# Optimization experiments

Measured on AMD Instinct MI355X. Metric: run time of the kernel, lower is better.

The kernel has to match this reference:

```python
import jax, jax.numpy as jnp
import numpy as np

# scipy.ndimage.gaussian_filter(sigma=1, truncate=4): radius 4, 9-tap kernel on EVERY axis
_R = 4
_xk = np.arange(-_R, _R + 1)
_wk = np.exp(-0.5 * _xk * _xk)
_W1D = (_wk / _wk.sum()).astype(np.float32)


def _sym_idx(n, r):
    # scipy 'reflect' (symmetric, edge repeated) extension indices for any r, any n
    p = np.arange(-r, n + r)
    q = np.mod(p, 2 * n)
    return np.where(q < n, q, 2 * n - 1 - q)


def gauss_filter(x):
    # separable sigma=1 Gaussian over ALL axes (incl. batch & channel), as scipy does
    w = jnp.asarray(_W1D)
    for axis in range(x.ndim):
        n = x.shape[axis]
        idx = jnp.asarray(_sym_idx(n, _R))
        xp = jnp.take(x, idx, axis=axis)  # symmetric-padded along `axis`
        acc = w[0] * jax.lax.slice_in_dim(xp, 0, n, axis=axis)
        for k in range(1, 2 * _R + 1):
            acc = acc + w[k] * jax.lax.slice_in_dim(xp, k, k + n, axis=axis)
        x = acc
    return x


def downsample(x):
    return x[:, :, ::2, ::2, ::2]


def upsample(x):
    # faithful to source: zero-interleave D and H, but zeros are APPENDED along W
    B, C, D, H, W = x.shape
    t = jnp.stack([x, jnp.zeros_like(x)], axis=3).reshape(B, C, 2 * D, H, W)
    t = jnp.stack([t, jnp.zeros_like(t)], axis=4).reshape(B, C, 2 * D, 2 * H, W)
    t = jnp.concatenate([t, jnp.zeros_like(t)], axis=4)  # (B,C,2D,2H,2W), 2nd W-half zero
    return gauss_filter(t * 8.0)


def lap_pyramid(img, max_levels):
    pyr = []
    cur = img
    for _ in range(max_levels):
        filt = gauss_filter(cur)
        down = downsample(filt)
        up = upsample(down)
        pyr.append(cur - up)
        cur = down
    return pyr


def setup_inputs():
    key = jax.random.key(0)
    k1, k2 = jax.random.split(key)
    shape = (2, 1, 64, 256, 256)
    return {
        "input": jax.random.normal(k1, shape, dtype=jnp.float32),
        "target": jax.random.normal(k2, shape, dtype=jnp.float32),
    }


def reference(input, target):
    max_levels = 5
    pyr_in = lap_pyramid(input, max_levels)
    pyr_tg = lap_pyramid(target, max_levels)
    loss = jnp.float32(0.0)
    for a, b in zip(pyr_in, pyr_tg):
        loss = loss + jnp.mean(jnp.abs(a - b))  # F.l1_loss (mean reduction)
    return loss
```

## Files before the change

### kernel.cpp

```cpp
#include <hip/hip_runtime.h>
#include <hip/hip_bf16.h>
#include <math.h>


struct GW { float w[9]; float A, B; };

__device__ __forceinline__ int ridx(int p, int n) {
    int m = 2 * n;
    int q = (p + m) & (m - 1);
    return (q < n) ? q : (m - 1 - q);
}

__device__ __forceinline__ float block_sum256(float v) {
    #pragma unroll
    for (int off = 32; off > 0; off >>= 1) v += __shfl_down(v, off, 64);
    __shared__ float wp[4];
    int tid = threadIdx.x;
    if ((tid & 63) == 0) wp[tid >> 6] = v;
    __syncthreads();
    return wp[0] + wp[1] + wp[2] + wp[3];
}

__device__ __forceinline__ float block_sum1024(float v) {
    #pragma unroll
    for (int off = 32; off > 0; off >>= 1) v += __shfl_down(v, off, 64);
    __shared__ float wp[16];
    int tid = threadIdx.x;
    if ((tid & 63) == 0) wp[tid >> 6] = v;
    __syncthreads();
    float t = 0.f;
    if (tid == 0) {
        #pragma unroll
        for (int w = 0; w < 16; ++w) t += wp[w];
    }
    return t;
}

template<bool WDIFF>
__global__ __launch_bounds__(256)
void k1l0(const float* __restrict__ in, const float* __restrict__ tg,
          float* __restrict__ T1, __hip_bfloat16* __restrict__ DIFF,
          float* __restrict__ P, GW g)
{
    const int H = 256, W = 256, Wd = 128;
    const int x0d = blockIdx.x * 64, y0d = blockIdx.y * 16, slice = blockIdx.z;
    __shared__ float raw[40][136];
    __shared__ float mid[40][64];
    const size_t in_off  = (size_t)slice * H * W;
    const size_t out_off = (size_t)slice * 128 * 128;
    const int tid = threadIdx.x;
    const int gy0 = 2*y0d - 4, gx0 = 2*x0d - 4;
    for (int i = tid; i < 40*32; i += 256) {
        int rr = i >> 5, c4 = (i & 31) + 1;
        int gy = ridx(gy0 + rr, H);
        size_t base = in_off + (size_t)gy * W + gx0 + 4*c4;
        float4 v = *(const float4*)(in + base);
        float4 b = *(const float4*)(tg + base);
        v.x -= b.x; v.y -= b.y; v.z -= b.z; v.w -= b.w;
        *(float4*)&raw[rr][4*c4] = v;
    }
    for (int i = tid; i < 40*8; i += 256) {
        int rr = i >> 3, j = i & 7;
        int cc = (j < 4) ? j : (128 + j);
        int gy = ridx(gy0 + rr, H);
        int gx = ridx(gx0 + cc, W);
        size_t idx = in_off + (size_t)gy * W + gx;
        raw[rr][cc] = in[idx] - tg[idx];
    }
    __syncthreads();
    if (WDIFF) {
        if (blockIdx.x == 0) {
            for (int i = tid; i < 32*128; i += 256) {
                int r = i >> 7, c = i & 127;
                DIFF[in_off + (size_t)(2*y0d + r) * W + c] =
                    __float2bfloat16(raw[4 + r][4 + c]);
            }
        } else {
            for (int i = tid; i < 32*4; i += 256) {
                int r = i >> 2, c = i & 3;
                DIFF[in_off + (size_t)(2*y0d + r) * W + 128 + c] =
                    __float2bfloat16(raw[4 + r][4 + c]);
            }
        }
    }
    if (blockIdx.x == 1) {
        float lsum = 0.f;
        for (int i = tid; i < 32*124; i += 256) {
            int r = i / 124, c = i - r*124;
            lsum += fabsf(raw[4 + r][8 + c]);
        }
        float tot = block_sum256(lsum);
        if (tid == 0)
            P[blockIdx.y + 8*blockIdx.z] = tot * (1.f / 8388608.f);
    }
    for (int i = tid; i < 40*64; i += 256) {
        int rr = i >> 6, c = i & 63;
        float s = 0.f;
        #pragma unroll
        for (int k = 0; k < 9; ++k) s = fmaf(g.w[k], raw[rr][2*c + k], s);
        mid[rr][c] = s;
    }
    __syncthreads();
    {
        int r = tid >> 6, c = tid & 63;
        int ox = x0d + c;
        #pragma unroll
        for (int j = 0; j < 4; ++j) {
            int oy = y0d + r*4 + j;
            int rb = 2*(r*4 + j);
            float s = 0.f;
            #pragma unroll
            for (int k = 0; k < 9; ++k) s = fmaf(g.w[k], mid[rb + k][c], s);
            T1[out_off + (size_t)oy * Wd + ox] = s;
        }
    }
}

__device__ void dev_k2_elem(long i, const float4* __restrict__ T, float4* __restrict__ O,
                            int D, int Dd, int M4, const GW& g)
{
    if (i >= (long)Dd * M4) return;
    int zd = (int)(i / M4);
    int q  = (int)(i - (long)zd * M4);
    float4 s0 = {0,0,0,0}, s1 = {0,0,0,0};
    #pragma unroll
    for (int k = 0; k < 9; ++k) {
        int zp = 2*zd - 4 + k;
        int zk = (zp >= 0 && zp < D) ? zp : ridx(zp, D);
        float4 a = T[(size_t)zk * M4 + q];
        float4 b = T[(size_t)(D + zk) * M4 + q];
        s0.x = fmaf(g.w[k], a.x, s0.x); s0.y = fmaf(g.w[k], a.y, s0.y);
        s0.z = fmaf(g.w[k], a.z, s0.z); s0.w = fmaf(g.w[k], a.w, s0.w);
        s1.x = fmaf(g.w[k], b.x, s1.x); s1.y = fmaf(g.w[k], b.y, s1.y);
        s1.z = fmaf(g.w[k], b.z, s1.z); s1.w = fmaf(g.w[k], b.w, s1.w);
    }
    float4 o0, o1;
    o0.x = g.A*s0.x + g.B*s1.x; o0.y = g.A*s0.y + g.B*s1.y;
    o0.z = g.A*s0.z + g.B*s1.z; o0.w = g.A*s0.w + g.B*s1.w;
    o1.x = g.B*s0.x + g.A*s1.x; o1.y = g.B*s0.y + g.A*s1.y;
    o1.z = g.B*s0.z + g.A*s1.z; o1.w = g.B*s0.w + g.A*s1.w;
    O[(size_t)zd * M4 + q] = o0;
    O[(size_t)(Dd + zd) * M4 + q] = o1;
}

__global__ __launch_bounds__(256)
void k2s(const float* __restrict__ Tin, float* __restrict__ Cout,
         int D, int Dd, int M4, GW g)
{
    long i = (long)blockIdx.x * 256 + threadIdx.x;
    dev_k2_elem(i, (const float4*)Tin, (float4*)Cout, D, Dd, M4, g);
}

__device__ void dev_k1_slice(const float* __restrict__ inA, float* __restrict__ out,
                             int x0d, int y0d, int slice, int H, int W, int Hd, int Wd,
                             const GW& g)
{
    __shared__ float raw[40][136];
    __shared__ float mid[40][64];
    const size_t in_off  = (size_t)slice * H * W;
    const size_t out_off = (size_t)slice * Hd * Wd;
    const int tid = threadIdx.x;
    const int gy0 = 2*y0d - 4, gx0 = 2*x0d - 4;
    if (2*x0d + 127 < W) {
        for (int i = tid; i < 40*32; i += 256) {
            int rr = i >> 5, c4 = (i & 31) + 1;
            int gy = ridx(gy0 + rr, H);
            *(float4*)&raw[rr][4*c4] =
                *(const float4*)(inA + in_off + (size_t)gy * W + gx0 + 4*c4);
        }
        for (int i = tid; i < 40*8; i += 256) {
            int rr = i >> 3, j = i & 7;
            int cc = (j < 4) ? j : (128 + j);
            int gy = ridx(gy0 + rr, H), gx = ridx(gx0 + cc, W);
            raw[rr][cc] = inA[in_off + (size_t)gy * W + gx];
        }
    } else {
        for (int i = tid; i < 40*136; i += 256) {
            int rr = i / 136, cc = i - rr*136;
            int gy = ridx(gy0 + rr, H), gx = ridx(gx0 + cc, W);
            raw[rr][cc] = inA[in_off + (size_t)gy * W + gx];
        }
    }
    __syncthreads();
    for (int i = tid; i < 40*64; i += 256) {
        int rr = i >> 6, c = i & 63;
        float s = 0.f;
        #pragma unroll
        for (int k = 0; k < 9; ++k) s = fmaf(g.w[k], raw[rr][2*c + k], s);
        mid[rr][c] = s;
    }
    __syncthreads();
    {
        int r = tid >> 6, c = tid & 63;
        int ox = x0d + c;
        #pragma unroll
        for (int j = 0; j < 4; ++j) {
            int oy = y0d + r*4 + j;
            if (oy < Hd && ox < Wd) {
                int rb = 2*(r*4 + j);
                float s = 0.f;
                #pragma unroll
                for (int k = 0; k < 9; ++k) s = fmaf(g.w[k], mid[rb + k][c], s);
                out[out_off + (size_t)oy * Wd + ox] = s;
            }
        }
    }
}

__device__ void dev_k3_elem(long i, const float4* __restrict__ Dn, float4* __restrict__ O,
                            int D, int Dd, int M4, const GW& g)
{
    if (i >= (long)D * M4) return;
    int z = (int)(i / M4);
    int q = (int)(i - (long)z * M4);
    float4 s0 = {0,0,0,0}, s1 = {0,0,0,0};
    auto f4 = [](float4& a, float w, const float4 b) {
        a.x = fmaf(w, b.x, a.x); a.y = fmaf(w, b.y, a.y);
        a.z = fmaf(w, b.z, a.z); a.w = fmaf(w, b.w, a.w);
    };
    if (z >= 4 && z + 4 < D) {
        if ((z & 1) == 0) {
            int base = (z >> 1) - 2;
            #pragma unroll
            for (int kk = 0; kk < 5; ++kk) {
                f4(s0, g.w[2*kk], Dn[(size_t)(base + kk) * M4 + q]);
                f4(s1, g.w[2*kk], Dn[(size_t)(Dd + base + kk) * M4 + q]);
            }
        } else {
            int base = (z - 3) >> 1;
            #pragma unroll
            for (int kk = 0; kk < 4; ++kk) {
                f4(s0, g.w[2*kk+1], Dn[(size_t)(base + kk) * M4 + q]);
                f4(s1, g.w[2*kk+1], Dn[(size_t)(Dd + base + kk) * M4 + q]);
            }
        }
    } else {
        #pragma unroll
        for (int k = 0; k < 9; ++k) {
            int zk = ridx(z - 4 + k, D);
            if (!(zk & 1)) {
                int j = zk >> 1;
                f4(s0, g.w[k], Dn[(size_t)j * M4 + q]);
                f4(s1, g.w[k], Dn[(size_t)(Dd + j) * M4 + q]);
            }
        }
    }
    float4 o0, o1;
    o0.x = 8.f*(g.A*s0.x + g.B*s1.x); o0.y = 8.f*(g.A*s0.y + g.B*s1.y);
    o0.z = 8.f*(g.A*s0.z + g.B*s1.z); o0.w = 8.f*(g.A*s0.w + g.B*s1.w);
    o1.x = 8.f*(g.B*s0.x + g.A*s1.x); o1.y = 8.f*(g.B*s0.y + g.A*s1.y);
    o1.z = 8.f*(g.B*s0.z + g.A*s1.z); o1.w = 8.f*(g.B*s0.w + g.A*s1.w);
    O[(size_t)z * M4 + q] = o0;
    O[(size_t)(D + z) * M4 + q] = o1;
}

__device__ void dev_k4v0(int local, const float* __restrict__ V0,
                         const __hip_bfloat16* __restrict__ DIFF,
                         const float* __restrict__ in, const float* __restrict__ tg,
                         int use_diff, float* __restrict__ P, const GW& g)
{
    __shared__ float vt[20][72];
    __shared__ float mid[20][64];
    const int H = 256, W = 256, Hd = 128, Wd = 128, Md = 128*128;
    const int s = local / 24;
    const int rem = local - s*24;
    const int ty = rem / 3, tx = rem - ty*3;
    const int x0 = tx*64, y0 = ty*32;
    const int tid = threadIdx.x;
    const int vy0 = (y0 >> 1) - 2;
    const size_t v_off = (size_t)s * Md;
    for (int i = tid; i < 20*72; i += 256) {
        int rr = i / 72, cc = i - rr*72;
        int vy = vy0 + rr;
        int txx = x0 - 4 + cc;
        if (txx < 0) txx = -1 - txx;
        float v = 0.f;
        if (vy >= 0 && vy < Hd && txx < Wd) v = V0[v_off + (size_t)vy * Wd + txx];
        vt[rr][cc] = v;
    }
    __syncthreads();
    for (int i = tid; i < 20*64; i += 256) {
        int rr = i >> 6, c = i & 63;
        float sv = 0.f;
        #pragma unroll
        for (int k = 0; k < 9; ++k) sv = fmaf(g.w[k], vt[rr][c + k], sv);
        mid[rr][c] = sv;
    }
    __syncthreads();
    const bool yin = (y0 >= 4) && (y0 + 35 < H);
    const int c = tid & 63;
    const int ry_base = (tid >> 6) * 8;
    const int ox = x0 + c;
    const size_t c_off = (size_t)s * H * W;
    float lsum = 0.f;
    #pragma unroll
    for (int j = 0; j < 8; ++j) {
        int ry = ry_base + j;
        int oy = y0 + ry;
        if (ox < 132 && oy < H) {
            float sv = 0.f;
            if (yin) {
                if (!(j & 1)) {
                    int r0 = ry >> 1;
                    sv = g.w[0]*mid[r0][c] + g.w[2]*mid[r0+1][c] + g.w[4]*mid[r0+2][c]
                       + g.w[6]*mid[r0+3][c] + g.w[8]*mid[r0+4][c];
                } else {
                    int r0 = ((ry - 3) >> 1) + 2;
                    sv = g.w[1]*mid[r0][c] + g.w[3]*mid[r0+1][c]
                       + g.w[5]*mid[r0+2][c] + g.w[7]*mid[r0+3][c];
                }
            } else {
                #pragma unroll
                for (int k = 0; k < 9; ++k) {
                    int gy = ridx(oy - 4 + k, H);
                    if (!(gy & 1)) sv = fmaf(g.w[k], mid[(gy >> 1) - vy0][c], sv);
                }
            }
            size_t idx = c_off + (size_t)oy * W + ox;
            float cv = use_diff ? __bfloat162float(DIFF[idx]) : (in[idx] - tg[idx]);
            lsum += fabsf(cv - sv);
        }
    }
    float tot = block_sum256(lsum);
    if (tid == 0) P[1024 + local] = tot * (1.f / 8388608.f);
}

__device__ void dev_k4f(int local, const float* __restrict__ dnb,
                        const float* __restrict__ cur, float* __restrict__ Pslot,
                        int D, int H, int ntx, int nty, float invn, const GW& g)
{
    __shared__ float vt[20][72];
    __shared__ float mid[20][64];
    const int W = H, Dd = D >> 1, Hd = H >> 1, Wd = W >> 1, Md = Hd * Wd;
    const int s = local / (ntx*nty);
    const int rem = local - s*(ntx*nty);
    const int ty = rem / ntx, tx = rem - ty*ntx;
    const int x0 = tx*64, y0 = ty*32;
    const int b = s / D, z = s - b*D;
    const float* dn0 = dnb + (size_t)b * Dd * Md;
    const float* dn1 = dnb + (size_t)(1 - b) * Dd * Md;
    const int tid = threadIdx.x;
    const int vy0 = (y0 >> 1) - 2;

    const bool zin = (z >= 4) && (z + 4 < D);
    if (zin && !(z & 1)) {
        const int j0 = (z >> 1) - 2;
        for (int i = tid; i < 20*72; i += 256) {
            int rr = i / 72, cc = i - rr*72;
            int vy = vy0 + rr;
            int txx = x0 - 4 + cc;
            if (txx < 0) txx = -1 - txx;
            float v = 0.f;
            if (vy >= 0 && vy < Hd && txx < Wd) {
                size_t o = (size_t)vy * Wd + txx;
                float s0 = 0.f, s1 = 0.f;
                #pragma unroll
                for (int t = 0; t < 5; ++t) {
                    s0 = fmaf(g.w[2*t], dn0[(size_t)(j0 + t) * Md + o], s0);
                    s1 = fmaf(g.w[2*t], dn1[(size_t)(j0 + t) * Md + o], s1);
                }
                v = 8.f * (g.A*s0 + g.B*s1);
            }
            vt[rr][cc] = v;
        }
    } else if (zin) {
        const int j0 = (z - 3) >> 1;
        for (int i = tid; i < 20*72; i += 256) {
            int rr = i / 72, cc = i - rr*72;
            int vy = vy0 + rr;
            int txx = x0 - 4 + cc;
            if (txx < 0) txx = -1 - txx;
            float v = 0.f;
            if (vy >= 0 && vy < Hd && txx < Wd) {
                size_t o = (size_t)vy * Wd + txx;
                float s0 = 0.f, s1 = 0.f;
                #pragma unroll
                for (int t = 0; t < 4; ++t) {
                    s0 = fmaf(g.w[2*t+1], dn0[(size_t)(j0 + t) * Md + o], s0);
                    s1 = fmaf(g.w[2*t+1], dn1[(size_t)(j0 + t) * Md + o], s1);
                }
                v = 8.f * (g.A*s0 + g.B*s1);
            }
            vt[rr][cc] = v;
        }
    } else {
        for (int i = tid; i < 20*72; i += 256) {
            int rr = i / 72, cc = i - rr*72;
            int vy = vy0 + rr;
            int txx = x0 - 4 + cc;
            if (txx < 0) txx = -1 - txx;
            float v = 0.f;
            if (vy >= 0 && vy < Hd && txx < Wd) {
                size_t o = (size_t)vy * Wd + txx;
                float s0 = 0.f, s1 = 0.f;
                #pragma unroll
                for (int k = 0; k < 9; ++k) {
                    int zk = ridx(z - 4 + k, D);
                    if (!(zk & 1)) {
                        int j = zk >> 1;
                        s0 = fmaf(g.w[k], dn0[(size_t)j * Md + o], s0);
                        s1 = fmaf(g.w[k], dn1[(size_t)j * Md + o], s1);
                    }
                }
                v = 8.f * (g.A*s0 + g.B*s1);
            }
            vt[rr][cc] = v;
        }
    }
    __syncthreads();
    for (int i = tid; i < 20*64; i += 256) {
        int rr = i >> 6, c = i & 63;
        float sv = 0.f;
        #pragma unroll
        for (int k = 0; k < 9; ++k) sv = fmaf(g.w[k], vt[rr][c + k], sv);
        mid[rr][c] = sv;
    }
    __syncthreads();
    const bool yin = (y0 >= 4) && (y0 + 35 < H);
    const int c = tid & 63;
    const int ry_base = (tid >> 6) * 8;
    const int ox = x0 + c;
    const size_t c_off = (size_t)s * H * W;
    float lsum = 0.f;
    #pragma unroll
    for (int j = 0; j < 8; ++j) {
        int ry = ry_base + j;
        int oy = y0 + ry;
        if (ox < W && oy < H) {
            float sv = 0.f;
            if (yin) {
                if (!(j & 1)) {
                    int r0 = ry >> 1;
                    sv = g.w[0]*mid[r0][c] + g.w[2]*mid[r0+1][c] + g.w[4]*mid[r0+2][c]
                       + g.w[6]*mid[r0+3][c] + g.w[8]*mid[r0+4][c];
                } else {
                    int r0 = ((ry - 3) >> 1) + 2;
                    sv = g.w[1]*mid[r0][c] + g.w[3]*mid[r0+1][c]
                       + g.w[5]*mid[r0+2][c] + g.w[7]*mid[r0+3][c];
                }
            } else {
                #pragma unroll
                for (int k = 0; k < 9; ++k) {
                    int gy = ridx(oy - 4 + k, H);
                    if (!(gy & 1)) sv = fmaf(g.w[k], mid[(gy >> 1) - vy0][c], sv);
                }
            }
            lsum += fabsf(cur[c_off + (size_t)oy * W + ox] - sv);
        }
    }
    float tot = block_sum256(lsum);
    if (tid == 0) Pslot[local] = tot * invn;
}

__global__ __launch_bounds__(256)
void kD3(const float* __restrict__ C1, float* __restrict__ Tl1,
         float* __restrict__ V0, GW g)
{
    int bid = (int)blockIdx.x;
    if (bid < 256) {
        int ty = bid & 3, slice = bid >> 2;
        dev_k1_slice(C1, Tl1, 0, ty*16, slice, 128, 128, 64, 64, g);
    } else {
        long i = (long)(bid - 256)*256 + threadIdx.x;
        dev_k3_elem(i, (const float4*)C1, (float4*)V0, 64, 32, 4096, g);
    }
}

__global__ __launch_bounds__(256)
void kD4(const float* __restrict__ Tl1, float* __restrict__ C2,
         const float* __restrict__ V0, const __hip_bfloat16* __restrict__ DIFF,
         const float* __restrict__ in, const float* __restrict__ tg,
         int use_diff, float* __restrict__ P, GW g)
{
    int bid = (int)blockIdx.x;
    if (bid < 64) {
        long i = (long)bid*256 + threadIdx.x;
        dev_k2_elem(i, (const float4*)Tl1, (float4*)C2, 32, 16, 1024, g);
    } else {
        dev_k4v0(bid - 64, V0, DIFF, in, tg, use_diff, P, g);
    }
}

__global__ __launch_bounds__(256)
void kD5(const float* __restrict__ C2, float* __restrict__ Tl2,
         const float* __restrict__ C1, float* __restrict__ P, GW g)
{
    int bid = (int)blockIdx.x;
    if (bid < 64) {
        int ty = bid & 1, slice = bid >> 1;
        dev_k1_slice(C2, Tl2, 0, ty*16, slice, 64, 64, 32, 32, g);
    } else {
        dev_k4f(bid - 64, C2, C1, P + 4096, 32, 128, 2, 4, 1.f / 1048576.f, g);
    }
}

__global__ __launch_bounds__(256)
void kD7(const float* __restrict__ C3, float* __restrict__ Tl3,
         const float* __restrict__ C2, float* __restrict__ P, GW g)
{
    int bid = (int)blockIdx.x;
    if (bid < 16) {
        dev_k1_slice(C3, Tl3, 0, 0, bid, 32, 32, 16, 16, g);
    } else {
        dev_k4f(bid - 16, C3, C2, P + 4608, 16, 64, 1, 2, 1.f / 131072.f, g);
    }
}

__global__ __launch_bounds__(256)
void kD9(const float* __restrict__ C4, float* __restrict__ Tl4,
         const float* __restrict__ C3, float* __restrict__ P, GW g)
{
    int bid = (int)blockIdx.x;
    if (bid < 8) {
        dev_k1_slice(C4, Tl4, 0, 0, bid, 16, 16, 8, 8, g);
    } else {
        dev_k4f(bid - 8, C4, C3, P + 4672, 8, 32, 1, 1, 1.f / 16384.f, g);
    }
}

__global__ __launch_bounds__(256)
void kD11(const float* __restrict__ C5, const float* __restrict__ C4,
          float* __restrict__ P, GW g)
{
    dev_k4f((int)blockIdx.x, C5, C4, P + 4688, 4, 16, 1, 1, 1.f / 2048.f, g);
}

__global__ __launch_bounds__(1024)
void kreduce(const float* __restrict__ P, int n, float* __restrict__ out)
{
    float s = 0.f;
    for (int i = threadIdx.x; i < n; i += 1024) s += P[i];
    float t = block_sum1024(s);
    if (threadIdx.x == 0) out[0] = t;
}

extern "C" void kernel_launch(void* const* d_in, const int* in_sizes, int n_in,
                              void* d_out, int out_size, void* d_ws, size_t ws_size,
                              hipStream_t stream)
{
    const float* in = (const float*)d_in[0];
    const float* tg = (const float*)d_in[1];
    float* out = (float*)d_out;

    GW g;
    {
        double u[9], S = 0.0;
        for (int k = 0; k < 9; ++k) { double d = k - 4; u[k] = exp(-0.5 * d * d); S += u[k]; }
        for (int k = 0; k < 9; ++k) g.w[k] = (float)(u[k] / S);
        g.A = (float)((2.0*u[0] + u[1] + u[3] + u[4]) / S);
        g.B = (float)((u[1] + 2.0*u[2] + u[3]) / S);
    }

    float* T1  = (float*)d_ws;
    float* C1  = T1  + 2097152;
    float* C2  = C1  + 1048576;
    float* C3  = C2  + 131072;
    float* C4  = C3  + 16384;
    float* C5  = C4  + 2048;
    float* Tl1 = C5  + 256;
    float* Tl2 = Tl1 + 262144;
    float* Tl3 = Tl2 + 32768;
    float* Tl4 = Tl3 + 4096;
    float* V0  = Tl4 + 512;
    float* P   = V0  + 2097152;
    float* wend = P + 8192;
    __hip_bfloat16* DIFF = (__hip_bfloat16*)wend;
    const size_t base_bytes = (size_t)((char*)wend - (char*)d_ws);
    const size_t diff_bytes = (size_t)2 * 64 * 256 * 256 * sizeof(__hip_bfloat16);
    const int use_diff = (ws_size >= base_bytes + diff_bytes) ? 1 : 0;

    dim3 blk(256);

    if (use_diff) k1l0<true ><<<dim3(2,8,128), blk, 0, stream>>>(in, tg, T1, DIFF, P, g);
    else          k1l0<false><<<dim3(2,8,128), blk, 0, stream>>>(in, tg, T1, nullptr, P, g);

    k2s<<<dim3(512), blk, 0, stream>>>(T1, C1, 64, 32, 4096, g);

    kD3<<<dim3(1280), blk, 0, stream>>>(C1, Tl1, V0, g);

    kD4<<<dim3(3136), blk, 0, stream>>>(Tl1, C2, V0, use_diff ? DIFF : nullptr,
                                        in, tg, use_diff, P, g);

    kD5<<<dim3(576), blk, 0, stream>>>(C2, Tl2, C1, P, g);

    k2s<<<dim3(8), blk, 0, stream>>>(Tl2, C3, 16, 8, 256, g);

    kD7<<<dim3(80), blk, 0, stream>>>(C3, Tl3, C2, P, g);

    k2s<<<dim3(1), blk, 0, stream>>>(Tl3, C4, 8, 4, 64, g);

    kD9<<<dim3(24), blk, 0, stream>>>(C4, Tl4, C3, P, g);

    k2s<<<dim3(1), blk, 0, stream>>>(Tl4, C5, 4, 2, 16, g);

    kD11<<<dim3(8), blk, 0, stream>>>(C5, C4, P, g);

    kreduce<<<dim3(1), dim3(1024), 0, stream>>>(P, 4696, out);
}
```

Baseline: 108.1 us.

## Fuse the last four pyramid-tail kernels into one shared-memory kernel

Four small tail launches (two z-downsample passes, a level-4 slice kernel and the level-5 loss kernel) become one 24-block kernel. Each block recomputes C4 from Tl3 in shared memory, and the level-5 blocks also rebuild Tl4 and C5 locally. This removes launch overhead and the serialization between tiny kernels, at the cost of redundant per-block work. dev_k4f now takes shared-memory pointers, so its __restrict__ qualifiers were dropped.

```diff
diff --git a/kernel.cpp b/kernel.cpp
--- a/kernel.cpp
+++ b/kernel.cpp
@@ -325,8 +325,8 @@
     if (tid == 0) P[1024 + local] = tot * (1.f / 8388608.f);
 }
 
-__device__ void dev_k4f(int local, const float* __restrict__ dnb,
-                        const float* __restrict__ cur, float* __restrict__ Pslot,
+__device__ void dev_k4f(int local, const float* dnb,
+                        const float* cur, float* Pslot,
                         int D, int H, int ntx, int nty, float invn, const GW& g)
 {
     __shared__ float vt[20][72];
@@ -507,22 +507,64 @@
 }
 
 __global__ __launch_bounds__(256)
-void kD9(const float* __restrict__ C4, float* __restrict__ Tl4,
-         const float* __restrict__ C3, float* __restrict__ P, GW g)
-{
-    int bid = (int)blockIdx.x;
-    if (bid < 8) {
-        dev_k1_slice(C4, Tl4, 0, 0, bid, 16, 16, 8, 8, g);
-    } else {
-        dev_k4f(bid - 8, C4, C3, P + 4672, 8, 32, 1, 1, 1.f / 16384.f, g);
-    }
-}
-
-__global__ __launch_bounds__(256)
-void kD11(const float* __restrict__ C5, const float* __restrict__ C4,
-          float* __restrict__ P, GW g)
-{
-    dev_k4f((int)blockIdx.x, C5, C4, P + 4688, 4, 16, 1, 1, 1.f / 2048.f, g);
+void tailpar(const float* __restrict__ Tl3g, const float* __restrict__ C3,
+             float* __restrict__ P, GW g)
+{
+    __shared__ float sTl3[4096];
+    __shared__ float sC4[2048];
+    __shared__ float sTl4[512];
+    __shared__ float sC5[256];
+    const int tid = threadIdx.x;
+    const int bid = (int)blockIdx.x;
+    for (int i = tid; i < 4096; i += 256) sTl3[i] = Tl3g[i];
+    __syncthreads();
+    for (int i = tid; i < 2048; i += 256) {
+        int slice = i >> 8, yx = i & 255;
+        int b = slice >> 2, zc = slice & 3;
+        float s0 = 0.f, s1 = 0.f;
+        #pragma unroll
+        for (int k = 0; k < 9; ++k) {
+            int zk = ridx(2*zc - 4 + k, 8);
+            s0 = fmaf(g.w[k], sTl3[zk*256 + yx], s0);
+            s1 = fmaf(g.w[k], sTl3[(8 + zk)*256 + yx], s1);
+        }
+        sC4[i] = (b == 0) ? (g.A*s0 + g.B*s1) : (g.B*s0 + g.A*s1);
+    }
+    __syncthreads();
+    if (bid < 16) {
+        dev_k4f(bid, sC4, C3, P + 4672, 8, 32, 1, 1, 1.f / 16384.f, g);
+    } else {
+        for (int i = tid; i < 512; i += 256) {
+            int slice = i >> 6, y = (i >> 3) & 7, x = i & 7;
+            float s = 0.f;
+            for (int ky = 0; ky < 9; ++ky) {
+                int gy = ridx(2*y - 4 + ky, 16);
+                float rs = 0.f;
+                #pragma unroll
+                for (int kx = 0; kx < 9; ++kx) {
+                    int gx = ridx(2*x - 4 + kx, 16);
+                    rs = fmaf(g.w[kx], sC4[slice*256 + gy*16 + gx], rs);
+                }
+                s = fmaf(g.w[ky], rs, s);
+            }
+            sTl4[i] = s;
+        }
+        __syncthreads();
+        for (int i = tid; i < 256; i += 256) {
+            int slice = i >> 6, yx = i & 63;
+            int b = slice >> 1, zc = slice & 1;
+            float s0 = 0.f, s1 = 0.f;
+            #pragma unroll
+            for (int k = 0; k < 9; ++k) {
+                int zk = ridx(2*zc - 4 + k, 4);
+                s0 = fmaf(g.w[k], sTl4[zk*64 + yx], s0);
+                s1 = fmaf(g.w[k], sTl4[(4 + zk)*64 + yx], s1);
+            }
+            sC5[i] = (b == 0) ? (g.A*s0 + g.B*s1) : (g.B*s0 + g.A*s1);
+        }
+        __syncthreads();
+        dev_k4f(bid - 16, sC5, sC4, P + 4688, 4, 16, 1, 1, 1.f / 2048.f, g);
+    }
 }
 
 __global__ __launch_bounds__(1024)
@@ -555,13 +597,10 @@
     float* C1  = T1  + 2097152;
     float* C2  = C1  + 1048576;
     float* C3  = C2  + 131072;
-    float* C4  = C3  + 16384;
-    float* C5  = C4  + 2048;
-    float* Tl1 = C5  + 256;
+    float* Tl1 = C3  + 16384;
     float* Tl2 = Tl1 + 262144;
     float* Tl3 = Tl2 + 32768;
-    float* Tl4 = Tl3 + 4096;
-    float* V0  = Tl4 + 512;
+    float* V0  = Tl3 + 4096;
     float* P   = V0  + 2097152;
     float* wend = P + 8192;
     __hip_bfloat16* DIFF = (__hip_bfloat16*)wend;
@@ -587,13 +626,7 @@
 
     kD7<<<dim3(80), blk, 0, stream>>>(C3, Tl3, C2, P, g);
 
-    k2s<<<dim3(1), blk, 0, stream>>>(Tl3, C4, 8, 4, 64, g);
-
-    kD9<<<dim3(24), blk, 0, stream>>>(C4, Tl4, C3, P, g);
-
-    k2s<<<dim3(1), blk, 0, stream>>>(Tl4, C5, 4, 2, 16, g);
-
-    kD11<<<dim3(8), blk, 0, stream>>>(C5, C4, P, g);
+    tailpar<<<dim3(24), blk, 0, stream>>>(Tl3, C3, P, g);
 
     kreduce<<<dim3(1), dim3(1024), 0, stream>>>(P, 4696, out);
 }
```

New measurement: 98.67 us (median of 2 runs). 1.1x faster.
